# Kernel tuning notes

Measured on AMD Instinct MI355X. Metric: run time of the kernel, lower is better.

Reference implementation:

```python
import jax, jax.numpy as jnp
import numpy as np

D = 14          # AOI image size (pixels per side)
K, B, F = 2, 512, 512   # spots, AOI batch, frame batch
N_T, N_F = 512, 1024    # total targets, total frames in target_locs table


def setup_inputs() -> dict:
    key = jax.random.key(0)
    ks = jax.random.split(key, 8)
    height = jax.random.uniform(ks[0], (K, B, F), dtype=jnp.float32) * 3000.0
    width = jax.random.uniform(ks[1], (K, B, F), dtype=jnp.float32) + 1.0  # keep > 0
    x = jax.random.normal(ks[2], (K, B, F), dtype=jnp.float32)
    y = jax.random.normal(ks[3], (K, B, F), dtype=jnp.float32)
    background = jax.random.uniform(ks[4], (B, F), dtype=jnp.float32) * 100.0
    target_locs = jax.random.normal(ks[5], (N_T, N_F, 2), dtype=jnp.float32) + (D - 1) / 2.0
    n_idx = jax.random.randint(ks[6], (B, 1), 0, N_T)
    f = jax.random.randint(ks[7], (F,), 0, N_F)
    return {"height": height, "width": width, "x": x, "y": y,
            "background": background, "target_locs": target_locs,
            "n_idx": n_idx, "f": f}


def reference(height, width, x, y, background, target_locs, n_idx, f):
    # spot centers: target_locs[n_idx, f] broadcasts [B,1] x [F] -> [B,F,2]
    locs = target_locs[n_idx, f]                 # [B, F, 2]
    sx = locs[..., 0] + x                        # [K, B, F] (i-coordinate)
    sy = locs[..., 1] + y                        # [K, B, F] (j-coordinate)
    pix = jnp.arange(D, dtype=height.dtype)      # [D]
    # separable squared distances (avoids a [K,B,F,D,D,2] intermediate)
    dx2 = (pix - sx[..., None]) ** 2             # [K, B, F, D]
    dy2 = (pix - sy[..., None]) ** 2             # [K, B, F, D]
    w2 = width * width                           # [K, B, F]
    # isotropic MVN density: exp(-r^2/(2 w^2)) / (2*pi*w^2)
    logp = (-jnp.log(2.0 * jnp.pi * w2)[..., None, None]
            - (dx2[..., :, None] + dy2[..., None, :]) / (2.0 * w2)[..., None, None])
    gaussian_spot = jnp.exp(logp)                # [K, B, F, D, D]
    img = (height[..., None, None] * gaussian_spot).sum(axis=0, keepdims=True)  # [1,B,F,D,D]
    return img + background[None, ..., None, None]
```

## Files before the change

kernel.cpp:

```cpp
#include <hip/hip_runtime.h>
#include <math.h>


#define DD 14
#define BB 512
#define FFRAMES 512
#define NF_TAB 1024
#define PAIRS_PER_BLOCK 64
#define BLOCK 256

__global__ __launch_bounds__(BLOCK) void gauss_spot_kernel(
    const float* __restrict__ height, const float* __restrict__ width,
    const float* __restrict__ xoff, const float* __restrict__ yoff,
    const float* __restrict__ background, const float* __restrict__ target_locs,
    const int* __restrict__ n_idx, const int* __restrict__ f_tab,
    float* __restrict__ out)
{
    __shared__ float lds[PAIRS_PER_BLOCK][4][DD];
    __shared__ float bg_s[PAIRS_PER_BLOCK];

    const int tid = threadIdx.x;
    const int pair_local = tid >> 2;
    const int sel = tid & 3;
    const int k = sel >> 1;
    const int isY = sel & 1;
    const int pair = blockIdx.x * PAIRS_PER_BLOCK + pair_local;
    const int b = pair >> 9;
    const int fi = pair & (FFRAMES - 1);

    const int n = n_idx[b];
    const int ff = f_tab[fi];
    const float loc = target_locs[(n * NF_TAB + ff) * 2 + isY];
    const int idx = k * (BB * FFRAMES) + pair;
    const float w = width[idx];
    const float off = isY ? yoff[idx] : xoff[idx];
    const float s = loc + off;
    const float inv2w2 = 1.0f / (2.0f * w * w);
    const float coef = isY ? 1.0f : height[idx] * inv2w2 * 0.31830988618379067f;
    const float a = inv2w2 * 1.4426950408889634f;

    #pragma unroll
    for (int i = 0; i < DD; ++i) {
        float d = (float)i - s;
        lds[pair_local][sel][i] = coef * exp2f(-d * d * a);
    }
    if (sel == 0) bg_s[pair_local] = background[pair];
    __syncthreads();

    float4* outv = (float4*)(out + (size_t)blockIdx.x * (PAIRS_PER_BLOCK * DD * DD));
    const int NV = PAIRS_PER_BLOCK * DD * DD / 4;
    for (int v = tid; v < NV; v += BLOCK) {
        int p = v / 49;
        int pix0 = (v - p * 49) * 4;
        float bg = bg_s[p];
        float4 r;
        #pragma unroll
        for (int e = 0; e < 4; ++e) {
            int pix = pix0 + e;
            int i = pix / DD;
            int j = pix - i * DD;
            ((float*)&r)[e] = bg
                + lds[p][0][i] * lds[p][1][j]
                + lds[p][2][i] * lds[p][3][j];
        }
        outv[v] = r;
    }
}

extern "C" void kernel_launch(void* const* d_in, const int* in_sizes, int n_in,
                              void* d_out, int out_size, void* d_ws, size_t ws_size,
                              hipStream_t stream) {
    const float* height      = (const float*)d_in[0];
    const float* width       = (const float*)d_in[1];
    const float* x           = (const float*)d_in[2];
    const float* y           = (const float*)d_in[3];
    const float* background  = (const float*)d_in[4];
    const float* target_locs = (const float*)d_in[5];
    const int*   n_idx       = (const int*)d_in[6];
    const int*   f           = (const int*)d_in[7];
    float* out = (float*)d_out;

    const int total_pairs = BB * FFRAMES;
    const int grid = total_pairs / PAIRS_PER_BLOCK;
    gauss_spot_kernel<<<grid, BLOCK, 0, stream>>>(
        height, width, x, y, background, target_locs, n_idx, f, out);
}
```

Measured before the change: 222.5 us.

## Compute image quarters in registers per thread, stage to LDS, then copy out

Each of the four threads per (B,F) pair now computes both spots' Gaussian factors in registers: all 14 y-factors and the 4 x-rows its quarter of the image needs. It writes 49 finished pixels to a shared image buffer. A plain vectorized LDS-to-global copy loop then replaces the old per-pixel divide/modulo indexing and the per-pixel LDS factor reads. This removes index arithmetic and scattered LDS reads, at the cost of redundant exp2 work, since each thread recomputes the y-factors, and more registers and LDS (about 50KB per block), which may lower occupancy.

```diff
diff --git a/kernel.cpp b/kernel.cpp
--- a/kernel.cpp
+++ b/kernel.cpp
@@ -8,6 +8,7 @@
 #define NF_TAB 1024
 #define PAIRS_PER_BLOCK 64
 #define BLOCK 256
+#define IMG (DD * DD)
 
 __global__ __launch_bounds__(BLOCK) void gauss_spot_kernel(
     const float* __restrict__ height, const float* __restrict__ width,
@@ -16,54 +17,73 @@
     const int* __restrict__ n_idx, const int* __restrict__ f_tab,
     float* __restrict__ out)
 {
-    __shared__ float lds[PAIRS_PER_BLOCK][4][DD];
-    __shared__ float bg_s[PAIRS_PER_BLOCK];
+    __shared__ float img[PAIRS_PER_BLOCK * IMG];
 
     const int tid = threadIdx.x;
-    const int pair_local = tid >> 2;
-    const int sel = tid & 3;
-    const int k = sel >> 1;
-    const int isY = sel & 1;
-    const int pair = blockIdx.x * PAIRS_PER_BLOCK + pair_local;
+    const int p = tid >> 2;
+    const int q = tid & 3;
+    const int pair = blockIdx.x * PAIRS_PER_BLOCK + p;
     const int b = pair >> 9;
     const int fi = pair & (FFRAMES - 1);
 
     const int n = n_idx[b];
     const int ff = f_tab[fi];
-    const float loc = target_locs[(n * NF_TAB + ff) * 2 + isY];
-    const int idx = k * (BB * FFRAMES) + pair;
-    const float w = width[idx];
-    const float off = isY ? yoff[idx] : xoff[idx];
-    const float s = loc + off;
-    const float inv2w2 = 1.0f / (2.0f * w * w);
-    const float coef = isY ? 1.0f : height[idx] * inv2w2 * 0.31830988618379067f;
-    const float a = inv2w2 * 1.4426950408889634f;
+    const float lx = target_locs[(n * NF_TAB + ff) * 2 + 0];
+    const float ly = target_locs[(n * NF_TAB + ff) * 2 + 1];
+    const float bg = background[pair];
 
+    const int i_lo = (49 * q) / 14;
+
+    float ex[2][4], ey[2][14];
     #pragma unroll
-    for (int i = 0; i < DD; ++i) {
-        float d = (float)i - s;
-        lds[pair_local][sel][i] = coef * exp2f(-d * d * a);
+    for (int k = 0; k < 2; ++k) {
+        const int idx = k * (BB * FFRAMES) + pair;
+        const float w = width[idx];
+        const float h = height[idx];
+        const float sx = lx + xoff[idx];
+        const float sy = ly + yoff[idx];
+        const float inv2w2 = 1.0f / (2.0f * w * w);
+        const float coef = h * inv2w2 * 0.31830988618379067f;
+        const float a = inv2w2 * 1.4426950408889634f;
+        #pragma unroll
+        for (int t = 0; t < 4; ++t) {
+            float d = (float)(i_lo + t) - sx;
+            ex[k][t] = coef * exp2f(-d * d * a);
+        }
+        #pragma unroll
+        for (int j = 0; j < 14; ++j) {
+            float d = (float)j - sy;
+            ey[k][j] = exp2f(-d * d * a);
+        }
     }
-    if (sel == 0) bg_s[pair_local] = background[pair];
+
+    float* dst = img + p * IMG + 49 * q;
+    if (q & 1) {
+        #pragma unroll
+        for (int e = 0; e < 49; ++e) {
+            const int il = (7 + e) / 14, j = (7 + e) % 14;
+            dst[e] = bg + ex[0][il] * ey[0][j] + ex[1][il] * ey[1][j];
+        }
+    } else {
+        #pragma unroll
+        for (int e = 0; e < 49; ++e) {
+            const int il = e / 14, j = e % 14;
+            dst[e] = bg + ex[0][il] * ey[0][j] + ex[1][il] * ey[1][j];
+        }
+    }
     __syncthreads();
 
-    float4* outv = (float4*)(out + (size_t)blockIdx.x * (PAIRS_PER_BLOCK * DD * DD));
-    const int NV = PAIRS_PER_BLOCK * DD * DD / 4;
-    for (int v = tid; v < NV; v += BLOCK) {
-        int p = v / 49;
-        int pix0 = (v - p * 49) * 4;
-        float bg = bg_s[p];
-        float4 r;
-        #pragma unroll
-        for (int e = 0; e < 4; ++e) {
-            int pix = pix0 + e;
-            int i = pix / DD;
-            int j = pix - i * DD;
-            ((float*)&r)[e] = bg
-                + lds[p][0][i] * lds[p][1][j]
-                + lds[p][2][i] * lds[p][3][j];
-        }
-        outv[v] = r;
+    const float4* src4 = (const float4*)img;
+    float4* out4 = (float4*)(out + (size_t)blockIdx.x * (PAIRS_PER_BLOCK * IMG));
+    const int NV = PAIRS_PER_BLOCK * IMG / 4;
+    #pragma unroll
+    for (int it = 0; it < 12; ++it) {
+        const int v = tid + it * BLOCK;
+        out4[v] = src4[v];
+    }
+    if (tid < NV - 12 * BLOCK) {
+        const int v = tid + 12 * BLOCK;
+        out4[v] = src4[v];
     }
 }
 
```

New measurement: 222.9 us. No clear change (+0.2%).
